# Performance work log

Hardware: AMD Instinct MI355X
Metric: run time of the kernel (lower is better)

## Reference

```python
import jax, jax.numpy as jnp
import numpy as np

IN_DIM = 8192
OUT_DIM = 8192
BATCH = 2048


def setup_inputs() -> dict:
    key = jax.random.key(0)
    k1, k2, k3, k4 = jax.random.split(key, 4)
    x = jax.random.uniform(k1, (BATCH, IN_DIM), dtype=jnp.float32)  # soft bits in [0,1]
    weights = jax.random.normal(k2, (OUT_DIM, 16), dtype=jnp.float32)
    idx_a = jax.random.randint(k3, (OUT_DIM,), 0, IN_DIM, dtype=jnp.int64)
    idx_b = jax.random.randint(k4, (OUT_DIM,), 0, IN_DIM, dtype=jnp.int64)
    return {"x": x, "weights": weights, "idx_a": idx_a, "idx_b": idx_b}


def _gate_values(a, b):
    # The 16 real-valued relaxations of the 2-input binary logic gates.
    ab = a * b
    return [
        jnp.zeros_like(a),      # 0:  False
        ab,                     # 1:  a AND b
        a - ab,                 # 2:  a AND NOT b
        a,                      # 3:  a
        b - ab,                 # 4:  NOT a AND b
        b,                      # 5:  b
        a + b - 2.0 * ab,       # 6:  a XOR b
        a + b - ab,             # 7:  a OR b
        1.0 - (a + b - ab),     # 8:  NOT (a OR b)
        1.0 - (a + b - 2.0 * ab),  # 9: NOT (a XOR b)
        1.0 - b,                # 10: NOT b
        1.0 - b + ab,           # 11: a OR NOT b
        1.0 - a,                # 12: NOT a
        1.0 - a + ab,           # 13: NOT a OR b
        1.0 - ab,               # 14: NOT (a AND b)
        jnp.ones_like(a),       # 15: True
    ]


def reference(x, weights, idx_a, idx_b):
    # training=True path of LogicLayer.forward_python
    a = x[:, idx_a]  # [B, OUT]
    b = x[:, idx_b]  # [B, OUT]
    w = jax.nn.softmax(weights, axis=-1)  # [OUT, 16]
    gates = _gate_values(a, b)
    out = jnp.zeros_like(a)
    for k in range(16):  # fixed small structural loop over the 16 gates
        out = out + w[None, :, k] * gates[k]
    return out
```

## Files before the change

kernel.cpp:

```cpp
#include <hip/hip_runtime.h>
#include <hip/hip_fp16.h>

#define IN_DIM 8192
#define OUT_DIM 8192
#define BATCH 2048
#define TPB 256
#define NIT (OUT_DIM / 4 / TPB)
#define NSTG (IN_DIM / 4 / TPB)

typedef float fvec4 __attribute__((ext_vector_type(4)));

#define GLOAD_LDS16(gp, lp)                                                        \
    __builtin_amdgcn_global_load_lds(                                              \
        (const __attribute__((address_space(1))) unsigned int*)(gp),               \
        (__attribute__((address_space(3))) unsigned int*)(lp), 16, 0, 0)

__global__ __launch_bounds__(64) void coeff_kernel(
    const float* __restrict__ w,
    const int* __restrict__ idx_a,
    const int* __restrict__ idx_b,
    int* __restrict__ pidx,
    float2* __restrict__ pcA,
    float2* __restrict__ pcB)
{
    int j = blockIdx.x * 64 + threadIdx.x;

    const float4* w4 = (const float4*)(w + (size_t)j * 16);
    float4 q0 = w4[0], q1 = w4[1], q2 = w4[2], q3 = w4[3];
    float wv[16] = { q0.x, q0.y, q0.z, q0.w,
                     q1.x, q1.y, q1.z, q1.w,
                     q2.x, q2.y, q2.z, q2.w,
                     q3.x, q3.y, q3.z, q3.w };

    float m = -1e30f;
#pragma unroll
    for (int k = 0; k < 16; ++k) m = fmaxf(m, wv[k]);
    float s = 0.f;
#pragma unroll
    for (int k = 0; k < 16; ++k) { wv[k] = __expf(wv[k] - m); s += wv[k]; }
    float inv = 1.0f / s;
#pragma unroll
    for (int k = 0; k < 16; ++k) wv[k] *= inv;

    float c0  = wv[8] + wv[9] + wv[10] + wv[11] + wv[12] + wv[13] + wv[14] + wv[15];
    float ca  = wv[2] + wv[3] + wv[6] + wv[7] - wv[8] - wv[9] - wv[12] - wv[13];
    float cb  = wv[4] + wv[5] + wv[6] + wv[7] - wv[8] - wv[9] - wv[10] - wv[11];
    float cab = wv[1] - wv[2] - wv[4] - 2.f * wv[6] - wv[7]
              + wv[8] + 2.f * wv[9] + wv[11] + wv[13] - wv[14];

    pidx[j] = ((idx_a[j] << 2) & 0xffff) | (idx_b[j] << 18);
    pcA[j]  = make_float2(c0, ca);
    pcB[j]  = make_float2(cb, cab);
}

__global__ __launch_bounds__(TPB, 5) void logic_kernel(
    const float* __restrict__ x,
    const int* __restrict__ pidx,
    const float2* __restrict__ pcA,
    const float2* __restrict__ pcB,
    float* __restrict__ out)
{
    __shared__ float xrow[IN_DIM];

    const int row = blockIdx.x;
    const int tid = threadIdx.x;

    const float* xr = x + (size_t)row * IN_DIM;
#pragma unroll
    for (int i = 0; i < NSTG; ++i)
        GLOAD_LDS16(xr + 4 * (i * TPB + tid), xrow + 4 * (i * TPB + tid));

    asm volatile("" ::: "memory");

    const int4*   pidx4 = (const int4*)pidx;
    const float4* pA4   = (const float4*)pcA;
    const float4* pB4   = (const float4*)pcB;

    int4   pi  = pidx4[tid];
    float4 cA0 = pA4[2 * tid],     cA1 = pA4[2 * tid + 1];
    float4 cB0 = pB4[2 * tid],     cB1 = pB4[2 * tid + 1];

    asm volatile("s_waitcnt vmcnt(5)" ::: "memory");
    __builtin_amdgcn_s_barrier();

    fvec4* out4 = (fvec4*)(out + (size_t)row * OUT_DIM);
    const char* xb = (const char*)xrow;

#pragma unroll
    for (int it = 0; it < NIT; ++it) {
        int4 pin = pi; float4 cA0n = cA0, cA1n = cA1, cB0n = cB0, cB1n = cB1;
        if (it + 1 < NIT) {
            int j4 = (it + 1) * TPB + tid;
            pin  = pidx4[j4];
            cA0n = pA4[2 * j4];     cA1n = pA4[2 * j4 + 1];
            cB0n = pB4[2 * j4];     cB1n = pB4[2 * j4 + 1];
        }

        float a0 = *(const float*)(xb + (pi.x & 0xffff)), b0 = *(const float*)(xb + ((unsigned)pi.x >> 16));
        float a1 = *(const float*)(xb + (pi.y & 0xffff)), b1 = *(const float*)(xb + ((unsigned)pi.y >> 16));
        float a2 = *(const float*)(xb + (pi.z & 0xffff)), b2 = *(const float*)(xb + ((unsigned)pi.z >> 16));
        float a3 = *(const float*)(xb + (pi.w & 0xffff)), b3 = *(const float*)(xb + ((unsigned)pi.w >> 16));

        fvec4 o;
        o.x = fmaf(fmaf(cB0.y, a0, cB0.x), b0, fmaf(cA0.y, a0, cA0.x));
        o.y = fmaf(fmaf(cB0.w, a1, cB0.z), b1, fmaf(cA0.w, a1, cA0.z));
        o.z = fmaf(fmaf(cB1.y, a2, cB1.x), b2, fmaf(cA1.y, a2, cA1.x));
        o.w = fmaf(fmaf(cB1.w, a3, cB1.z), b3, fmaf(cA1.w, a3, cA1.z));
        __builtin_nontemporal_store(o, &out4[it * TPB + tid]);

        pi = pin; cA0 = cA0n; cA1 = cA1n; cB0 = cB0n; cB1 = cB1n;
    }
}

extern "C" void kernel_launch(void* const* d_in, const int* in_sizes, int n_in,
                              void* d_out, int out_size, void* d_ws, size_t ws_size,
                              hipStream_t stream)
{
    const float* x       = (const float*)d_in[0];
    const float* weights = (const float*)d_in[1];
    const int*   idx_a   = (const int*)d_in[2];
    const int*   idx_b   = (const int*)d_in[3];
    float* out = (float*)d_out;

    int*    pidx = (int*)d_ws;
    float2* pcA  = (float2*)(pidx + OUT_DIM);
    float2* pcB  = pcA + OUT_DIM;

    coeff_kernel<<<OUT_DIM / 64, 64, 0, stream>>>(weights, idx_a, idx_b, pidx, pcA, pcB);
    logic_kernel<<<BATCH, TPB, 0, stream>>>(x, pidx, pcA, pcB, out);
}
```

Baseline: 124.5 us.

## Process four rows per block with double-buffered LDS row prefetch

Each block now handles four batch rows using 512 threads. The packed indices and coefficients are loaded into registers once and reused across all four rows. The next x row is prefetched into a second LDS buffer while the current row is being computed. The aim is to amortise coefficient loads and overlap row staging with compute, at the cost of more LDS and registers per block, fewer blocks, and lower occupancy.

```diff
diff --git a/kernel.cpp b/kernel.cpp
--- a/kernel.cpp
+++ b/kernel.cpp
@@ -4,8 +4,9 @@
 #define IN_DIM 8192
 #define OUT_DIM 8192
 #define BATCH 2048
-#define TPB 256
-#define NIT (OUT_DIM / 4 / TPB)
+#define TPB 512
+#define RPB 4
+#define NQ (OUT_DIM / 4 / TPB)
 #define NSTG (IN_DIM / 4 / TPB)
 
 typedef float fvec4 __attribute__((ext_vector_type(4)));
@@ -53,62 +54,77 @@
     pcB[j]  = make_float2(cb, cab);
 }
 
-__global__ __launch_bounds__(TPB, 5) void logic_kernel(
+__global__ __launch_bounds__(TPB, 4) void logic_kernel(
     const float* __restrict__ x,
     const int* __restrict__ pidx,
     const float2* __restrict__ pcA,
     const float2* __restrict__ pcB,
     float* __restrict__ out)
 {
-    __shared__ float xrow[IN_DIM];
+    __shared__ float xrow[2][IN_DIM];
 
-    const int row = blockIdx.x;
-    const int tid = threadIdx.x;
-
-    const float* xr = x + (size_t)row * IN_DIM;
-#pragma unroll
-    for (int i = 0; i < NSTG; ++i)
-        GLOAD_LDS16(xr + 4 * (i * TPB + tid), xrow + 4 * (i * TPB + tid));
-
-    asm volatile("" ::: "memory");
+    const int tid  = threadIdx.x;
+    const int row0 = blockIdx.x * RPB;
 
     const int4*   pidx4 = (const int4*)pidx;
     const float4* pA4   = (const float4*)pcA;
     const float4* pB4   = (const float4*)pcB;
 
-    int4   pi  = pidx4[tid];
-    float4 cA0 = pA4[2 * tid],     cA1 = pA4[2 * tid + 1];
-    float4 cB0 = pB4[2 * tid],     cB1 = pB4[2 * tid + 1];
+    int4   pi[NQ];
+    float4 cA[2 * NQ];
+    float4 cB[2 * NQ];
+#pragma unroll
+    for (int q = 0; q < NQ; ++q) {
+        int j4 = q * TPB + tid;
+        pi[q]         = pidx4[j4];
+        cA[2 * q]     = pA4[2 * j4];
+        cA[2 * q + 1] = pA4[2 * j4 + 1];
+        cB[2 * q]     = pB4[2 * j4];
+        cB[2 * q + 1] = pB4[2 * j4 + 1];
+    }
 
-    asm volatile("s_waitcnt vmcnt(5)" ::: "memory");
-    __builtin_amdgcn_s_barrier();
-
-    fvec4* out4 = (fvec4*)(out + (size_t)row * OUT_DIM);
-    const char* xb = (const char*)xrow;
+    {
+        const float* xr = x + (size_t)row0 * IN_DIM;
+#pragma unroll
+        for (int i = 0; i < NSTG; ++i)
+            GLOAD_LDS16(xr + 4 * (i * TPB + tid), &xrow[0][4 * (i * TPB + tid)]);
+    }
 
 #pragma unroll
-    for (int it = 0; it < NIT; ++it) {
-        int4 pin = pi; float4 cA0n = cA0, cA1n = cA1, cB0n = cB0, cB1n = cB1;
-        if (it + 1 < NIT) {
-            int j4 = (it + 1) * TPB + tid;
-            pin  = pidx4[j4];
-            cA0n = pA4[2 * j4];     cA1n = pA4[2 * j4 + 1];
-            cB0n = pB4[2 * j4];     cB1n = pB4[2 * j4 + 1];
+    for (int r = 0; r < RPB; ++r) {
+        if (r == 0) asm volatile("s_waitcnt vmcnt(0)" ::: "memory");
+        else        asm volatile("s_waitcnt vmcnt(4)" ::: "memory");
+        __builtin_amdgcn_s_barrier();
+
+        if (r + 1 < RPB) {
+            const float* xn = x + (size_t)(row0 + r + 1) * IN_DIM;
+#pragma unroll
+            for (int i = 0; i < NSTG; ++i)
+                GLOAD_LDS16(xn + 4 * (i * TPB + tid), &xrow[(r + 1) & 1][4 * (i * TPB + tid)]);
         }
+        asm volatile("" ::: "memory");
 
-        float a0 = *(const float*)(xb + (pi.x & 0xffff)), b0 = *(const float*)(xb + ((unsigned)pi.x >> 16));
-        float a1 = *(const float*)(xb + (pi.y & 0xffff)), b1 = *(const float*)(xb + ((unsigned)pi.y >> 16));
-        float a2 = *(const float*)(xb + (pi.z & 0xffff)), b2 = *(const float*)(xb + ((unsigned)pi.z >> 16));
-        float a3 = *(const float*)(xb + (pi.w & 0xffff)), b3 = *(const float*)(xb + ((unsigned)pi.w >> 16));
+        const char* xb = (const char*)xrow[r & 1];
+        fvec4* out4 = (fvec4*)(out + (size_t)(row0 + r) * OUT_DIM);
 
-        fvec4 o;
-        o.x = fmaf(fmaf(cB0.y, a0, cB0.x), b0, fmaf(cA0.y, a0, cA0.x));
-        o.y = fmaf(fmaf(cB0.w, a1, cB0.z), b1, fmaf(cA0.w, a1, cA0.z));
-        o.z = fmaf(fmaf(cB1.y, a2, cB1.x), b2, fmaf(cA1.y, a2, cA1.x));
-        o.w = fmaf(fmaf(cB1.w, a3, cB1.z), b3, fmaf(cA1.w, a3, cA1.z));
-        __builtin_nontemporal_store(o, &out4[it * TPB + tid]);
+#pragma unroll
+        for (int q = 0; q < NQ; ++q) {
+            int4 p = pi[q];
+            float a0 = *(const float*)(xb + (p.x & 0xffff)), b0 = *(const float*)(xb + ((unsigned)p.x >> 16));
+            float a1 = *(const float*)(xb + (p.y & 0xffff)), b1 = *(const float*)(xb + ((unsigned)p.y >> 16));
+            float a2 = *(const float*)(xb + (p.z & 0xffff)), b2 = *(const float*)(xb + ((unsigned)p.z >> 16));
+            float a3 = *(const float*)(xb + (p.w & 0xffff)), b3 = *(const float*)(xb + ((unsigned)p.w >> 16));
 
-        pi = pin; cA0 = cA0n; cA1 = cA1n; cB0 = cB0n; cB1 = cB1n;
+            float4 A0 = cA[2 * q], A1 = cA[2 * q + 1];
+            float4 B0 = cB[2 * q], B1 = cB[2 * q + 1];
+
+            fvec4 o;
+            o.x = fmaf(fmaf(B0.y, a0, B0.x), b0, fmaf(A0.y, a0, A0.x));
+            o.y = fmaf(fmaf(B0.w, a1, B0.z), b1, fmaf(A0.w, a1, A0.z));
+            o.z = fmaf(fmaf(B1.y, a2, B1.x), b2, fmaf(A1.y, a2, A1.x));
+            o.w = fmaf(fmaf(B1.w, a3, B1.z), b3, fmaf(A1.w, a3, A1.z));
+            __builtin_nontemporal_store(o, &out4[q * TPB + tid]);
+        }
     }
 }
 
@@ -127,5 +143,5 @@
     float2* pcB  = pcA + OUT_DIM;
 
     coeff_kernel<<<OUT_DIM / 64, 64, 0, stream>>>(weights, idx_a, idx_b, pidx, pcA, pcB);
-    logic_kernel<<<BATCH, TPB, 0, stream>>>(x, pidx, pcA, pcB, out);
+    logic_kernel<<<BATCH / RPB, TPB, 0, stream>>>(x, pidx, pcA, pcB, out);
 }
```

New measurement: 119.2 us. -4.3%, faster.
